# Optimization experiments

Measured on AMD Instinct MI355X. Metric: run time of the kernel, lower is better.

The kernel has to match this reference:

```python
import jax, jax.numpy as jnp
import numpy as np

N_NODES = 10000
N_EDGES = 80000
IN_DIM = 768
HID = 256
HEADS = 8
NEG_SLOPE = 0.2


def setup_inputs() -> dict:
    key = jax.random.key(0)
    ks = jax.random.split(key, 12)
    s = 0.02
    x = jax.random.normal(ks[0], (N_NODES, IN_DIM), dtype=jnp.float32)
    edge_index = jax.random.randint(ks[1], (2, N_EDGES), 0, N_NODES, dtype=jnp.int64)
    W1 = jax.random.normal(ks[2], (IN_DIM, HEADS * HID), dtype=jnp.float32) * s
    a_src1 = jax.random.normal(ks[3], (HEADS, HID), dtype=jnp.float32) * s
    a_dst1 = jax.random.normal(ks[4], (HEADS, HID), dtype=jnp.float32) * s
    b1 = jnp.zeros((HEADS * HID,), dtype=jnp.float32)
    W2 = jax.random.normal(ks[5], (HEADS * HID, HEADS * HID), dtype=jnp.float32) * s
    a_src2 = jax.random.normal(ks[6], (HEADS, HID), dtype=jnp.float32) * s
    a_dst2 = jax.random.normal(ks[7], (HEADS, HID), dtype=jnp.float32) * s
    b2 = jnp.zeros((HID,), dtype=jnp.float32)
    # graph_projection: 256 -> 256
    Wp = jax.random.normal(ks[8], (HID, HID), dtype=jnp.float32) * s
    bp = jnp.zeros((HID,), dtype=jnp.float32)
    return dict(x=x, edge_index=edge_index, W1=W1, a_src1=a_src1, a_dst1=a_dst1,
                b1=b1, W2=W2, a_src2=a_src2, a_dst2=a_dst2, b2=b2, Wp=Wp, bp=bp)


def _gat_conv(x, src, dst, W, a_src, a_dst, b, concat):
    """PyG GATConv (eval mode, self-loops already appended to src/dst)."""
    N = x.shape[0]
    H, C = a_src.shape
    h = (x @ W).reshape(N, H, C)                         # [N,H,C] per-head projection
    alpha_s = jnp.sum(h * a_src[None], axis=-1)           # [N,H]
    alpha_d = jnp.sum(h * a_dst[None], axis=-1)           # [N,H]
    e = jax.nn.leaky_relu(alpha_s[src] + alpha_d[dst], NEG_SLOPE)  # [E,H]
    # segment softmax over incoming edges of each dst node
    m = jax.ops.segment_max(e, dst, num_segments=N)       # [N,H]
    m = jnp.where(jnp.isfinite(m), m, 0.0)
    p = jnp.exp(e - m[dst])
    denom = jax.ops.segment_sum(p, dst, num_segments=N)   # [N,H]
    alpha = p / (denom[dst] + 1e-16)                      # [E,H]
    out = jax.ops.segment_sum(alpha[:, :, None] * h[src], dst, num_segments=N)  # [N,H,C]
    if concat:
        return out.reshape(N, H * C) + b
    return out.mean(axis=1) + b


def reference(x, edge_index, W1, a_src1, a_dst1, b1, W2, a_src2, a_dst2, b2, Wp, bp):
    N = x.shape[0]
    loops = jnp.arange(N, dtype=edge_index.dtype)
    src = jnp.concatenate([edge_index[0], loops])
    dst = jnp.concatenate([edge_index[1], loops])
    h = _gat_conv(x, src, dst, W1, a_src1, a_dst1, b1, concat=True)   # [N, 2048]
    h = jax.nn.elu(h)                                                 # dropout: eval/no-op
    h = _gat_conv(h, src, dst, W2, a_src2, a_dst2, b2, concat=False)  # [N, 256]
    h = h @ Wp + bp
    return jax.nn.relu(h)                                             # dropout: eval/no-op
```

## Files before the change

### kernel.cpp

```cpp
#include <hip/hip_runtime.h>
#include <cstdint>
#include <cstddef>

#define IN_DIM  768
#define NNODES  10000
#define MPAD    10112
#define NEDGES  80000
#define E_TOT   90000
#define HEADS   8
#define HID     256
#define HC      2048
#define NEG_SLOPE 0.2f

#define CVT_BLK  ((MPAD * IN_DIM / 4) / 256)
#define CNT_BLK  ((E_TOT + 255) / 256)
#define T1_BLK   ((HC / 32) * (IN_DIM / 32))
#define T2_BLK   ((HC / 32) * (HC / 32))
#define TP_BLK   ((HID / 32) * (HID / 32))
#define PREP_BLK (CVT_BLK + CNT_BLK + T1_BLK + T2_BLK + TP_BLK)

typedef _Float16 __attribute__((ext_vector_type(8))) f16x8;
typedef float    __attribute__((ext_vector_type(4))) f32x4;

__device__ __forceinline__ int edge_src(const int* __restrict__ ei, int e) {
    return (e < NEDGES) ? ei[e] : (e - NEDGES);
}
__device__ __forceinline__ int edge_dst(const int* __restrict__ ei, int e) {
    return (e < NEDGES) ? ei[NEDGES + e] : (e - NEDGES);
}

__device__ __forceinline__ void tcvt_body(
    const float* __restrict__ W, _Float16* __restrict__ T,
    int K, int N, int bx, int by, int t)
{
    __shared__ float tile[32][33];
    int tx = t & 31, ty = t >> 5;
#pragma unroll
    for (int q = 0; q < 4; q++)
        tile[ty + q * 8][tx] = W[(size_t)(by * 32 + ty + q * 8) * N + bx * 32 + tx];
    __syncthreads();
#pragma unroll
    for (int q = 0; q < 4; q++) {
        float v = tile[tx][ty + q * 8];
        T[(size_t)(bx * 32 + ty + q * 8) * K + by * 32 + tx] = (_Float16)v;
    }
}

__global__ __launch_bounds__(256) void prep_kernel(
    const float* __restrict__ x, _Float16* __restrict__ xh,
    const int* __restrict__ ei, int* __restrict__ cnt,
    const float* __restrict__ W1, _Float16* __restrict__ W1t,
    const float* __restrict__ W2, _Float16* __restrict__ W2t,
    const float* __restrict__ Wp, _Float16* __restrict__ Wpt)
{
    int b = blockIdx.x;
    int t = threadIdx.x;
    if (b < CVT_BLK) {
        int i = b * 256 + t;
        size_t e = (size_t)i * 4;
        int r = (int)(e / IN_DIM);
        float4 v = (r < NNODES) ? *(const float4*)(x + e)
                                : make_float4(0.f, 0.f, 0.f, 0.f);
        _Float16 h4[4] = {(_Float16)v.x, (_Float16)v.y, (_Float16)v.z, (_Float16)v.w};
        *(ushort4*)(xh + e) = *(ushort4*)h4;
    } else if (b < CVT_BLK + CNT_BLK) {
        int e = (b - CVT_BLK) * 256 + t;
        if (e < E_TOT) atomicAdd(&cnt[edge_dst(ei, e)], 1);
    } else if (b < CVT_BLK + CNT_BLK + T1_BLK) {
        int idx = b - (CVT_BLK + CNT_BLK);
        tcvt_body(W1, W1t, IN_DIM, HC, idx % (HC / 32), idx / (HC / 32), t);
    } else if (b < CVT_BLK + CNT_BLK + T1_BLK + T2_BLK) {
        int idx = b - (CVT_BLK + CNT_BLK + T1_BLK);
        tcvt_body(W2, W2t, HC, HC, idx % (HC / 32), idx / (HC / 32), t);
    } else {
        int idx = b - (CVT_BLK + CNT_BLK + T1_BLK + T2_BLK);
        tcvt_body(Wp, Wpt, HID, HID, idx % (HID / 32), idx / (HID / 32), t);
    }
}

__global__ void scan_kernel(const int* __restrict__ cnt, int* __restrict__ indptr) {
    __shared__ int sums[1024];
    const int CH = 10;
    int t = threadIdx.x;
    int base = t * CH;
    int s = 0;
#pragma unroll
    for (int i = 0; i < CH; i++) { int idx = base + i; if (idx < NNODES) s += cnt[idx]; }
    sums[t] = s;
    __syncthreads();
    for (int off = 1; off < 1024; off <<= 1) {
        int v = (t >= off) ? sums[t - off] : 0;
        __syncthreads();
        sums[t] += v;
        __syncthreads();
    }
    int run = (t == 0) ? 0 : sums[t - 1];
#pragma unroll
    for (int i = 0; i < CH; i++) {
        int idx = base + i;
        if (idx < NNODES) { indptr[idx] = run; run += cnt[idx]; }
    }
    if (t == 0) indptr[NNODES] = E_TOT;
}

__global__ void scatter_kernel(const int* __restrict__ ei, const int* __restrict__ indptr,
                               int* __restrict__ cur, int* __restrict__ sorted) {
    int e = blockIdx.x * 256 + threadIdx.x;
    if (e < E_TOT) {
        int d = edge_dst(ei, e);
        int pos = atomicAdd(&cur[d], 1);
        sorted[indptr[d] + pos] = e;
    }
}

template <int EPI>
__global__ __launch_bounds__(256) void mfma_gemm_kernel(
    const _Float16* __restrict__ A, const _Float16* __restrict__ B,
    void* __restrict__ Cout, const float* __restrict__ bias,
    int M, int K, int Nn, int swz)
{
    __shared__ __align__(16) _Float16 sA[2][128 * 32];
    __shared__ __align__(16) _Float16 sB[2][128 * 32];

    int t = threadIdx.x;
    int bx = blockIdx.x, by = blockIdx.y;
    if (swz) {
        int id = by * 16 + bx;
        int xcd = id & 7, slot = id >> 3;
        bx = 2 * xcd + (slot & 1);
        by = slot >> 1;
    }
    int row0 = by * 128;
    int col0 = bx * 128;

    int s0 = t, s1 = t + 256;
    int m0 = s0 >> 2, k0 = (s0 & 3) * 8;
    int m1 = s1 >> 2, k1 = (s1 & 3) * 8;
    const _Float16* a0 = A + (size_t)(row0 + m0) * K + k0;
    const _Float16* a1 = A + (size_t)(row0 + m1) * K + k1;
    const _Float16* b0 = B + (size_t)(col0 + m0) * K + k0;
    const _Float16* b1 = B + (size_t)(col0 + m1) * K + k1;

    int w = t >> 6, lane = t & 63;
    int wm = (w & 1) * 64, wn = (w >> 1) * 64;
    int fr = lane & 15, quad = lane >> 4;

    auto stage = [&](int kt, int bsel) {
        _Float16* dA0 = &sA[bsel][(w * 64) * 8];
        _Float16* dA1 = &sA[bsel][(w * 64 + 256) * 8];
        _Float16* dB0 = &sB[bsel][(w * 64) * 8];
        _Float16* dB1 = &sB[bsel][(w * 64 + 256) * 8];
        __builtin_amdgcn_global_load_lds(
            (const __attribute__((address_space(1))) void*)(a0 + kt),
            (__attribute__((address_space(3))) void*)dA0, 16, 0, 0);
        __builtin_amdgcn_global_load_lds(
            (const __attribute__((address_space(1))) void*)(a1 + kt),
            (__attribute__((address_space(3))) void*)dA1, 16, 0, 0);
        __builtin_amdgcn_global_load_lds(
            (const __attribute__((address_space(1))) void*)(b0 + kt),
            (__attribute__((address_space(3))) void*)dB0, 16, 0, 0);
        __builtin_amdgcn_global_load_lds(
            (const __attribute__((address_space(1))) void*)(b1 + kt),
            (__attribute__((address_space(3))) void*)dB1, 16, 0, 0);
    };

    f32x4 acc[4][4];
#pragma unroll
    for (int i = 0; i < 4; i++)
#pragma unroll
        for (int j = 0; j < 4; j++) acc[i][j] = {0.f, 0.f, 0.f, 0.f};

    const int nIt = K / 32;
    stage(0, 0);
    __syncthreads();

    for (int it = 0; it < nIt; ++it) {
        int cb = it & 1;
        if (it + 1 < nIt) stage((it + 1) * 32, cb ^ 1);

        f16x8 fa[4], fb[4];
#pragma unroll
        for (int i = 0; i < 4; i++) {
            fa[i] = *(const f16x8*)&sA[cb][(wm + i * 16 + fr) * 32 + quad * 8];
            fb[i] = *(const f16x8*)&sB[cb][(wn + i * 16 + fr) * 32 + quad * 8];
        }
#pragma unroll
        for (int i = 0; i < 4; i++)
#pragma unroll
            for (int j = 0; j < 4; j++)
                acc[i][j] = __builtin_amdgcn_mfma_f32_16x16x32_f16(fa[i], fb[j], acc[i][j], 0, 0, 0);

        if (it + 1 < nIt) __syncthreads();
    }

    if (EPI == 0) {
        _Float16* C = (_Float16*)Cout;
#pragma unroll
        for (int i = 0; i < 4; i++) {
            int mbase = row0 + wm + i * 16 + quad * 4;
#pragma unroll
            for (int j = 0; j < 4; j++) {
                int n = col0 + wn + j * 16 + fr;
#pragma unroll
                for (int r = 0; r < 4; r++) {
                    int m = mbase + r;
                    if (m < M) C[(size_t)m * Nn + n] = (_Float16)acc[i][j][r];
                }
            }
        }
    } else {
        float* C = (float*)Cout;
        float bv[4];
#pragma unroll
        for (int j = 0; j < 4; j++) bv[j] = bias[col0 + wn + j * 16 + fr];
#pragma unroll
        for (int i = 0; i < 4; i++) {
            int mbase = row0 + wm + i * 16 + quad * 4;
#pragma unroll
            for (int j = 0; j < 4; j++) {
                int n = col0 + wn + j * 16 + fr;
#pragma unroll
                for (int r = 0; r < 4; r++) {
                    int m = mbase + r;
                    if (m < M) C[(size_t)m * Nn + n] = fmaxf(acc[i][j][r] + bv[j], 0.f);
                }
            }
        }
    }
}

__global__ __launch_bounds__(256) void attn_kernel(
    const _Float16* __restrict__ H, const float* __restrict__ a_src,
    const float* __restrict__ a_dst, float* __restrict__ as_out,
    float* __restrict__ ad_out)
{
    int n = blockIdx.x;
    int t = threadIdx.x;
    int h = t >> 5, l = t & 31;
    f16x8 hv = *(const f16x8*)&H[(size_t)n * HC + h * HID + l * 8];
    const float* asp = a_src + h * HID + l * 8;
    const float* adp = a_dst + h * HID + l * 8;
    float sa = 0.f, sd = 0.f;
#pragma unroll
    for (int q = 0; q < 8; q++) {
        float v = (float)hv[q];
        sa = fmaf(v, asp[q], sa);
        sd = fmaf(v, adp[q], sd);
    }
#pragma unroll
    for (int o = 16; o > 0; o >>= 1) {
        sa += __shfl_xor(sa, o, 32);
        sd += __shfl_xor(sd, o, 32);
    }
    if (l == 0) { as_out[n * HEADS + h] = sa; ad_out[n * HEADS + h] = sd; }
}

template <int MODE>
__global__ __launch_bounds__(256) void agg_kernel(
    const _Float16* __restrict__ H, const float* __restrict__ as_,
    const float* __restrict__ ad_, const float* __restrict__ bias,
    const int* __restrict__ indptr, const int* __restrict__ sorted,
    const int* __restrict__ ei, _Float16* __restrict__ outh)
{
    __shared__ float m8[HEADS], d8[HEADS], adl[HEADS];
    __shared__ int   srcl[64];
    __shared__ float al[64][HEADS];
    __shared__ float red[HC];

    int n = blockIdx.x;
    int t = threadIdx.x;

    if (n >= NNODES) {
        if (MODE == 0) {
            _Float16 z8[8] = {};
            *(f16x8*)&outh[(size_t)n * HC + t * 8] = *(f16x8*)z8;
        } else {
            outh[(size_t)n * HID + t] = (_Float16)0.f;
        }
        return;
    }

    int start = indptr[n];
    int deg = indptr[n + 1] - start;

    if (t < HEADS) adl[t] = ad_[n * HEADS + t];
    __syncthreads();

    int h = t >> 5, l = t & 31;
    float adh = adl[h];

    float mx = -1e30f;
    for (int j = l; j < deg; j += 32) {
        int e = sorted[start + j];
        int s = edge_src(ei, e);
        float v = as_[s * HEADS + h] + adh;
        v = (v >= 0.f) ? v : NEG_SLOPE * v;
        mx = fmaxf(mx, v);
    }
#pragma unroll
    for (int o = 16; o > 0; o >>= 1) mx = fmaxf(mx, __shfl_xor(mx, o, 32));

    float sm = 0.f;
    for (int j = l; j < deg; j += 32) {
        int e = sorted[start + j];
        int s = edge_src(ei, e);
        float v = as_[s * HEADS + h] + adh;
        v = (v >= 0.f) ? v : NEG_SLOPE * v;
        sm += expf(v - mx);
    }
#pragma unroll
    for (int o = 16; o > 0; o >>= 1) sm += __shfl_xor(sm, o, 32);
    if (l == 0) { m8[h] = mx; d8[h] = sm; }

    int hh = t >> 5, c8 = (t & 31) * 8;
    const size_t hoff = (size_t)hh * HID + c8;
    float acc[8] = {};
    for (int base = 0; base < deg; base += 64) {
        int cntc = min(64, deg - base);
        __syncthreads();
        if (t < cntc) srcl[t] = edge_src(ei, sorted[start + base + t]);
        __syncthreads();
        {
            int j = t & 63, h0 = t >> 6;
            if (j < cntc) {
#pragma unroll
                for (int q = 0; q < 2; q++) {
                    int hx = h0 + q * 4;
                    float v = as_[srcl[j] * HEADS + hx] + adl[hx];
                    v = (v >= 0.f) ? v : NEG_SLOPE * v;
                    al[j][hx] = expf(v - m8[hx]) / (d8[hx] + 1e-16f);
                }
            }
        }
        __syncthreads();
        int jj = 0;
        for (; jj + 3 < cntc; jj += 4) {
            int sx0 = srcl[jj + 0], sx1 = srcl[jj + 1];
            int sx2 = srcl[jj + 2], sx3 = srcl[jj + 3];
            f16x8 h0v = *(const f16x8*)&H[(size_t)sx0 * HC + hoff];
            f16x8 h1v = *(const f16x8*)&H[(size_t)sx1 * HC + hoff];
            f16x8 h2v = *(const f16x8*)&H[(size_t)sx2 * HC + hoff];
            f16x8 h3v = *(const f16x8*)&H[(size_t)sx3 * HC + hoff];
            float a0 = al[jj + 0][hh], a1 = al[jj + 1][hh];
            float a2 = al[jj + 2][hh], a3 = al[jj + 3][hh];
#pragma unroll
            for (int q = 0; q < 8; q++) acc[q] = fmaf(a0, (float)h0v[q], acc[q]);
#pragma unroll
            for (int q = 0; q < 8; q++) acc[q] = fmaf(a1, (float)h1v[q], acc[q]);
#pragma unroll
            for (int q = 0; q < 8; q++) acc[q] = fmaf(a2, (float)h2v[q], acc[q]);
#pragma unroll
            for (int q = 0; q < 8; q++) acc[q] = fmaf(a3, (float)h3v[q], acc[q]);
        }
        for (; jj < cntc; jj++) {
            int s = srcl[jj];
            f16x8 hv = *(const f16x8*)&H[(size_t)s * HC + hoff];
            float a = al[jj][hh];
#pragma unroll
            for (int q = 0; q < 8; q++)
                acc[q] = fmaf(a, (float)hv[q], acc[q]);
        }
    }

    if (MODE == 0) {
        _Float16 o8[8];
#pragma unroll
        for (int q = 0; q < 8; q++) {
            float v = acc[q] + bias[hoff + q];
            v = (v > 0.f) ? v : expm1f(v);
            o8[q] = (_Float16)v;
        }
        *(f16x8*)&outh[(size_t)n * HC + hoff] = *(f16x8*)o8;
    } else {
#pragma unroll
        for (int q = 0; q < 8; q++) red[hoff + q] = acc[q];
        __syncthreads();
        float s = 0.f;
#pragma unroll
        for (int h2 = 0; h2 < HEADS; h2++) s += red[h2 * HID + t];
        outh[(size_t)n * HID + t] = (_Float16)(s * 0.125f + bias[t]);
    }
}

extern "C" void kernel_launch(void* const* d_in, const int* in_sizes, int n_in,
                              void* d_out, int out_size, void* d_ws, size_t ws_size,
                              hipStream_t stream)
{
    const float* x      = (const float*)d_in[0];
    const int*   ei     = (const int*)  d_in[1];
    const float* W1     = (const float*)d_in[2];
    const float* a_src1 = (const float*)d_in[3];
    const float* a_dst1 = (const float*)d_in[4];
    const float* b1     = (const float*)d_in[5];
    const float* W2     = (const float*)d_in[6];
    const float* a_src2 = (const float*)d_in[7];
    const float* a_dst2 = (const float*)d_in[8];
    const float* b2     = (const float*)d_in[9];
    const float* Wp     = (const float*)d_in[10];
    const float* bp     = (const float*)d_in[11];
    float* out = (float*)d_out;

    char* ws = (char*)d_ws;
    size_t off = 0;
    auto alloc = [&](size_t bytes) -> char* {
        char* p = ws + off;
        off += (bytes + 255) & ~(size_t)255;
        return p;
    };
    _Float16* Hbuf = (_Float16*)alloc((size_t)NNODES * HC * 2);
    _Float16* A2   = (_Float16*)alloc((size_t)MPAD * HC * 2);
    _Float16* W1t  = (_Float16*)alloc((size_t)HC * IN_DIM * 2);
    _Float16* W2t  = (_Float16*)alloc((size_t)HC * HC * 2);
    _Float16* Wpt  = (_Float16*)alloc((size_t)HID * HID * 2);
    _Float16* xh   = (_Float16*)alloc((size_t)MPAD * IN_DIM * 2);
    _Float16* out2h = (_Float16*)alloc((size_t)MPAD * HID * 2);
    float* asad   = (float*)alloc((size_t)4 * NNODES * HEADS * sizeof(float));
    float* as1 = asad;
    float* ad1 = asad + (size_t)NNODES * HEADS;
    float* as2 = asad + (size_t)2 * NNODES * HEADS;
    float* ad2 = asad + (size_t)3 * NNODES * HEADS;
    int*   cntcur = (int*)alloc((size_t)2 * NNODES * sizeof(int));
    int*   cnt = cntcur;
    int*   cur = cntcur + NNODES;
    int*   indptr = (int*)  alloc((size_t)(NNODES + 1) * sizeof(int));
    int*   sorted = (int*)  alloc((size_t)E_TOT * sizeof(int));

    hipMemsetAsync(cntcur, 0, (size_t)2 * NNODES * sizeof(int), stream);
    prep_kernel<<<PREP_BLK, 256, 0, stream>>>(x, xh, ei, cnt,
                                              W1, W1t, W2, W2t, Wp, Wpt);
    scan_kernel<<<1, 1024, 0, stream>>>(cnt, indptr);
    scatter_kernel<<<(E_TOT + 255) / 256, 256, 0, stream>>>(ei, indptr, cur, sorted);

    dim3 gMf(HC / 128, MPAD / 128);

    mfma_gemm_kernel<0><<<gMf, 256, 0, stream>>>(xh, W1t, Hbuf, nullptr,
                                                 NNODES, IN_DIM, HC, 1);
    attn_kernel<<<NNODES, 256, 0, stream>>>(Hbuf, a_src1, a_dst1, as1, ad1);
    agg_kernel<0><<<MPAD, 256, 0, stream>>>(Hbuf, as1, ad1, b1, indptr, sorted, ei, A2);

    mfma_gemm_kernel<0><<<gMf, 256, 0, stream>>>(A2, W2t, Hbuf, nullptr,
                                                 NNODES, HC, HC, 1);
    attn_kernel<<<NNODES, 256, 0, stream>>>(Hbuf, a_src2, a_dst2, as2, ad2);
    agg_kernel<1><<<MPAD, 256, 0, stream>>>(Hbuf, as2, ad2, b2, indptr, sorted, ei, out2h);

    dim3 gProj(HID / 128, MPAD / 128);
    mfma_gemm_kernel<1><<<gProj, 256, 0, stream>>>(out2h, Wpt, out, bp,
                                                   NNODES, HID, HID, 0);
}
```

Baseline: 452.9 us.

## Replace layer GEMMs with 256x256-tile 8-wave MFMA kernel using direct-to-LDS loads

Adds a new GEMM kernel with 256x256 output tiles, 512 threads (8 waves) and a K-step of 64. Operands are loaded straight into LDS with global_load_lds into a double buffer, using an XOR swizzle, and the compute is split into four quadrant phases that overlap the next stage's loads with MFMA work under barriers and raised priority. It also remaps workgroups across XCDs and pads MPAD to a multiple of 256. The larger tile is meant to raise operand reuse and hide memory latency for the two large layer GEMMs. In exchange it gives fewer workgroups (8x40), carries heavy register pressure, and has a fragile hand-written wait-count schedule.

New measurement: 481.5 us. 1.06x slower.

```diff
diff --git a/kernel.cpp b/kernel.cpp
--- a/kernel.cpp
+++ b/kernel.cpp
@@ -4,7 +4,7 @@
 
 #define IN_DIM  768
 #define NNODES  10000
-#define MPAD    10112
+#define MPAD    10240
 #define NEDGES  80000
 #define E_TOT   90000
 #define HEADS   8
@@ -111,6 +111,141 @@
         int pos = atomicAdd(&cur[d], 1);
         sorted[indptr[d] + pos] = e;
     }
+}
+
+__global__ __launch_bounds__(512, 2) void gemm8p_kernel(
+    const _Float16* __restrict__ A, const _Float16* __restrict__ B,
+    _Float16* __restrict__ C, int M, int K, int Nn)
+{
+    __shared__ __align__(16) _Float16 lds[2][4][128 * 64];
+
+    const int t = threadIdx.x;
+    const int w = t >> 6, lane = t & 63;
+    const int fr = lane & 15, q4 = lane >> 4;
+    const int wr = w >> 2, wc = w & 3;
+
+    const int nwgx = gridDim.x;
+    int wg = blockIdx.y * nwgx + blockIdx.x;
+    const int cpx = (nwgx * gridDim.y) >> 3;
+    wg = (wg & 7) * cpx + (wg >> 3);
+    const int row0 = (wg / nwgx) * 256;
+    const int col0 = (wg % nwgx) * 256;
+
+    const int srow0 = t >> 3,         sslot0 = t & 7;
+    const int srow1 = (t + 512) >> 3, sslot1 = (t + 512) & 7;
+    const int scol0 = (sslot0 ^ (srow0 & 7)) << 3;
+    const int scol1 = (sslot1 ^ (srow1 & 7)) << 3;
+    const int ldso0 = (w * 64) << 3;
+    const int ldso1 = (512 + w * 64) << 3;
+
+    auto stage = [&](int half, int kel, int bb) {
+        const _Float16* P;
+        int rbase;
+        if (half >= 2) { P = B; rbase = col0 + (half - 2) * 128; }
+        else           { P = A; rbase = row0 + half * 128; }
+        const _Float16* s0 = P + (size_t)(rbase + srow0) * K + kel + scol0;
+        const _Float16* s1 = P + (size_t)(rbase + srow1) * K + kel + scol1;
+        __builtin_amdgcn_global_load_lds(
+            (const __attribute__((address_space(1))) void*)s0,
+            (__attribute__((address_space(3))) void*)&lds[bb][half][ldso0], 16, 0, 0);
+        __builtin_amdgcn_global_load_lds(
+            (const __attribute__((address_space(1))) void*)s1,
+            (__attribute__((address_space(3))) void*)&lds[bb][half][ldso1], 16, 0, 0);
+    };
+
+    f32x4 acc[2][2][4][2];
+#pragma unroll
+    for (int qm = 0; qm < 2; qm++)
+#pragma unroll
+        for (int qn = 0; qn < 2; qn++)
+#pragma unroll
+            for (int mi = 0; mi < 4; mi++)
+#pragma unroll
+                for (int ni = 0; ni < 2; ni++)
+                    acc[qm][qn][mi][ni] = {0.f, 0.f, 0.f, 0.f};
+
+#define PHASE(QM, QN, BB, SH, KT1, DOSTAGE, VMN)                                \
+    do {                                                                        \
+        f16x8 fa[4][2], fb[2][2];                                               \
+        _Pragma("unroll")                                                       \
+        for (int mi = 0; mi < 4; mi++) {                                        \
+            _Pragma("unroll")                                                   \
+            for (int ks = 0; ks < 2; ks++) {                                    \
+                int lr = wr * 64 + mi * 16 + fr;                                \
+                int sl = ((ks << 2) | q4) ^ (fr & 7);                           \
+                fa[mi][ks] = *(const f16x8*)&lds[BB][QM][(lr << 6) + (sl << 3)];\
+            }                                                                   \
+        }                                                                       \
+        _Pragma("unroll")                                                       \
+        for (int ni = 0; ni < 2; ni++) {                                        \
+            _Pragma("unroll")                                                   \
+            for (int ks = 0; ks < 2; ks++) {                                    \
+                int lr = wc * 32 + ni * 16 + fr;                                \
+                int sl = ((ks << 2) | q4) ^ (fr & 7);                           \
+                fb[ni][ks] = *(const f16x8*)&lds[BB][2 + QN][(lr << 6) + (sl << 3)];\
+            }                                                                   \
+        }                                                                       \
+        if (DOSTAGE) stage(SH, KT1, (BB) ^ 1);                                  \
+        asm volatile("s_waitcnt vmcnt(" #VMN ")" ::: "memory");                 \
+        __builtin_amdgcn_s_barrier();                                           \
+        asm volatile("s_waitcnt lgkmcnt(0)" ::: "memory");                      \
+        __builtin_amdgcn_sched_barrier(0);                                      \
+        __builtin_amdgcn_s_setprio(1);                                          \
+        _Pragma("unroll")                                                       \
+        for (int ks = 0; ks < 2; ks++) {                                        \
+            _Pragma("unroll")                                                   \
+            for (int mi = 0; mi < 4; mi++) {                                    \
+                _Pragma("unroll")                                               \
+                for (int ni = 0; ni < 2; ni++)                                  \
+                    acc[QM][QN][mi][ni] = __builtin_amdgcn_mfma_f32_16x16x32_f16(\
+                        fa[mi][ks], fb[ni][ks], acc[QM][QN][mi][ni], 0, 0, 0);  \
+            }                                                                   \
+        }                                                                       \
+        __builtin_amdgcn_s_setprio(0);                                          \
+        __builtin_amdgcn_sched_barrier(0);                                      \
+        __builtin_amdgcn_s_barrier();                                           \
+    } while (0)
+
+    stage(0, 0, 0); stage(2, 0, 0); stage(3, 0, 0); stage(1, 0, 0);
+    asm volatile("s_waitcnt vmcnt(0)" ::: "memory");
+    __builtin_amdgcn_s_barrier();
+
+    const int nT = K >> 6;
+    int t0 = 0;
+    for (; t0 < nT - 1; ++t0) {
+        int bb = t0 & 1;
+        int kt1 = (t0 + 1) << 6;
+        PHASE(0, 0, bb, 0, kt1, 1, 4);
+        PHASE(0, 1, bb, 2, kt1, 1, 4);
+        PHASE(1, 0, bb, 3, kt1, 1, 4);
+        PHASE(1, 1, bb, 1, kt1, 1, 4);
+    }
+    {
+        int bb = t0 & 1;
+        PHASE(0, 0, bb, 0, 0, 0, 0);
+        PHASE(0, 1, bb, 0, 0, 0, 0);
+        PHASE(1, 0, bb, 0, 0, 0, 0);
+        PHASE(1, 1, bb, 0, 0, 0, 0);
+    }
+#undef PHASE
+
+#pragma unroll
+    for (int qm = 0; qm < 2; qm++)
+#pragma unroll
+        for (int qn = 0; qn < 2; qn++)
+#pragma unroll
+            for (int mi = 0; mi < 4; mi++) {
+                int mb = row0 + qm * 128 + wr * 64 + mi * 16 + q4 * 4;
+#pragma unroll
+                for (int ni = 0; ni < 2; ni++) {
+                    int n = col0 + qn * 128 + wc * 32 + ni * 16 + fr;
+#pragma unroll
+                    for (int r = 0; r < 4; r++) {
+                        int m = mb + r;
+                        if (m < M) C[(size_t)m * Nn + n] = (_Float16)acc[qm][qn][mi][ni][r];
+                    }
+                }
+            }
 }
 
 template <int EPI>
@@ -431,15 +566,13 @@
     scan_kernel<<<1, 1024, 0, stream>>>(cnt, indptr);
     scatter_kernel<<<(E_TOT + 255) / 256, 256, 0, stream>>>(ei, indptr, cur, sorted);
 
-    dim3 gMf(HC / 128, MPAD / 128);
-
-    mfma_gemm_kernel<0><<<gMf, 256, 0, stream>>>(xh, W1t, Hbuf, nullptr,
-                                                 NNODES, IN_DIM, HC, 1);
+    dim3 g8(HC / 256, MPAD / 256);
+
+    gemm8p_kernel<<<g8, 512, 0, stream>>>(xh, W1t, Hbuf, NNODES, IN_DIM, HC);
     attn_kernel<<<NNODES, 256, 0, stream>>>(Hbuf, a_src1, a_dst1, as1, ad1);
     agg_kernel<0><<<MPAD, 256, 0, stream>>>(Hbuf, as1, ad1, b1, indptr, sorted, ei, A2);
 
-    mfma_gemm_kernel<0><<<gMf, 256, 0, stream>>>(A2, W2t, Hbuf, nullptr,
-                                                 NNODES, HC, HC, 1);
+    gemm8p_kernel<<<g8, 512, 0, stream>>>(A2, W2t, Hbuf, NNODES, HC, HC);
     attn_kernel<<<NNODES, 256, 0, stream>>>(Hbuf, a_src2, a_dst2, as2, ad2);
     agg_kernel<1><<<MPAD, 256, 0, stream>>>(Hbuf, as2, ad2, b2, indptr, sorted, ei, out2h);
 
```
